# Kernel tuning notes

Hardware: AMD Instinct MI355X
Metric: run time of the kernel (lower is better)

The kernel has to match this reference:

```python
import jax, jax.numpy as jnp
import numpy as np

DEPTH = 3
MAX_NB = 10
HIDDEN = 128


def setup_inputs() -> dict:
    key = jax.random.key(0)
    k = jax.random.split(key, 14)
    B, A, E, H, NB = 64, 1024, 2048, HIDDEN, MAX_NB
    s = 0.05
    return {
        "input_atom": jax.random.normal(k[0], (B, A, 82), jnp.float32),
        "input_bond": jax.random.normal(k[1], (B, E, 6), jnp.float32),
        "atom_graph": jax.random.randint(k[2], (B, A, NB), 0, A),
        "bond_graph": jax.random.randint(k[3], (B, A, NB), 0, E),
        "num_nbs": jax.random.randint(k[4], (B, A), 0, NB + 1),
        "node_mask": jnp.ones((B, A), jnp.float32),
        "W_atom": jax.random.normal(k[5], (82, H), jnp.float32) * s,
        "W_nei_atom": jax.random.normal(k[6], (H, H), jnp.float32) * s,
        "W_nei_bond": jax.random.normal(k[7], (6, H), jnp.float32) * s,
        "W_self": jax.random.normal(k[8], (H, H), jnp.float32) * s,
        "W_U2": jax.random.normal(k[9], (H + 6, H), jnp.float32) * s,
        "b_U2": jax.random.normal(k[10], (H,), jnp.float32) * s,
        "W_U1": jax.random.normal(k[11], (2 * H, H), jnp.float32) * s,
        "b_U1": jax.random.normal(k[12], (H,), jnp.float32) * s,
    }


def reference(input_atom, input_bond, atom_graph, bond_graph, num_nbs, node_mask,
              W_atom, W_nei_atom, W_nei_bond, W_self, W_U2, b_U2, W_U1, b_U1):
    B, A, NB = atom_graph.shape
    H = W_atom.shape[1]
    atom_features = input_atom @ W_atom                       # [B, A, H]
    # neighbor validity mask: [B, A, NB, 1]
    mask_nei = (jnp.arange(NB)[None, None, :] < num_nbs[:, :, None]).astype(jnp.float32)[..., None]
    idx_a = atom_graph.reshape(B, A * NB, 1)
    idx_b = bond_graph.reshape(B, A * NB, 1)
    # bond neighbor features are loop-invariant: gather once
    fbond_nei = jnp.take_along_axis(input_bond, idx_b, axis=1).reshape(B, A, NB, 6)
    h_nei_bond = fbond_nei @ W_nei_bond                       # [B, A, NB, H]
    node_m = node_mask[..., None]                             # [B, A, 1]
    kernel = None
    for _ in range(DEPTH):
        fatom_nei = jnp.take_along_axis(atom_features, idx_a, axis=1).reshape(B, A, NB, H)
        h_nei = (fatom_nei @ W_nei_atom) * h_nei_bond         # [B, A, NB, H]
        f_nei = jnp.sum(h_nei * mask_nei, axis=2)             # [B, A, H]
        f_self = atom_features @ W_self                        # [B, A, H]
        kernel = f_nei * f_self * node_m
        l_nei = jnp.concatenate([fatom_nei, fbond_nei], axis=3)  # [B, A, NB, H+6]
        pre_label = l_nei @ W_U2 + b_U2
        nei_label = jnp.sum(pre_label * mask_nei, axis=2)      # [B, A, H]
        new_label = jnp.concatenate([atom_features, nei_label], axis=2)
        atom_features = new_label @ W_U1 + b_U1
    return kernel, atom_features
```

## Files before the change

### kernel.cpp

```cpp
#include <hip/hip_runtime.h>

constexpr int NB = 10, H = 128;
constexpr int M = 64 * 1024;
constexpr long SL = (long)M * H;

typedef __attribute__((ext_vector_type(8))) short s16x8;
typedef __attribute__((ext_vector_type(4))) float f32x4;

__device__ __forceinline__ ushort f2b(float f) {
    union { float f; uint u; } v; v.f = f;
    uint u = v.u;
    uint r = u + 0x7fffu + ((u >> 16) & 1u);
    return (ushort)(r >> 16);
}
__device__ __forceinline__ float b2f(ushort u) {
    union { uint u; float f; } v; v.u = ((uint)u) << 16; return v.f;
}

__device__ __forceinline__ int swz(int bid, int cpx) {
    return (bid & 7) * cpx + (bid >> 3);
}

template<int NC, int FLAGS>
__global__ __launch_bounds__(256, 4) void gemm_af(
    const ushort* __restrict__ Abf, const ushort* __restrict__ WT,
    const ushort* __restrict__ FNb, const float* __restrict__ nmask,
    float* __restrict__ Cf, ushort* __restrict__ Cb)
{
    constexpr bool KOUT = FLAGS & 8, OF32 = FLAGS & 16;
    constexpr int K = NC * 32;
    const int lane = threadIdx.x & 63, wid = threadIdx.x >> 6;
    const int l15 = lane & 15, g = lane >> 4;
    const int t0 = swz(blockIdx.x, 128) * 4;

    s16x8 w[2][NC];
    #pragma unroll
    for (int ct = 0; ct < 2; ++ct)
        #pragma unroll
        for (int kc = 0; kc < NC; ++kc)
            w[ct][kc] = *(const s16x8*)(WT + (size_t)((2 * wid + ct) * 16 + l15) * K + kc * 32 + g * 8);

    s16x8 ac[NC], an[NC];
    #pragma unroll
    for (int kc = 0; kc < NC; ++kc)
        ac[kc] = *(const s16x8*)(Abf + (size_t)(t0 * 16 + l15) * K + kc * 32 + g * 8);

    #pragma unroll
    for (int i = 0; i < 4; ++i) {
        const int m0 = (t0 + i) * 16;
        if (i < 3) {
            #pragma unroll
            for (int kc = 0; kc < NC; ++kc)
                an[kc] = *(const s16x8*)(Abf + (size_t)(m0 + 16 + l15) * K + kc * 32 + g * 8);
        }
        f32x4 acc[2];
        #pragma unroll
        for (int ct = 0; ct < 2; ++ct) acc[ct] = (f32x4){0.f, 0.f, 0.f, 0.f};
        #pragma unroll
        for (int kc = 0; kc < NC; ++kc)
            #pragma unroll
            for (int ct = 0; ct < 2; ++ct)
                acc[ct] = __builtin_amdgcn_mfma_f32_16x16x32_bf16(ac[kc], w[ct][kc], acc[ct], 0, 0, 0);

        #pragma unroll
        for (int ct = 0; ct < 2; ++ct) {
            const int col = (2 * wid + ct) * 16 + l15;
            #pragma unroll
            for (int r = 0; r < 4; ++r) {
                const int m = m0 + 4 * g + r;
                const size_t o = (size_t)m * H + col;
                float v = acc[ct][r];
                if constexpr (KOUT) v = v * b2f(FNb[o]) * nmask[m];
                if constexpr (OF32) Cf[o] = v; else Cb[o] = f2b(v);
            }
        }
        #pragma unroll
        for (int kc = 0; kc < NC; ++kc) ac[kc] = an[kc];
    }
}

template<bool OF32>
__global__ __launch_bounds__(256, 2) void u1f(
    const ushort* __restrict__ AF, const ushort* __restrict__ SATOM,
    const ushort* __restrict__ FBSb, const ushort* __restrict__ WT,
    float* __restrict__ Cf, ushort* __restrict__ Cb)
{
    const int lane = threadIdx.x & 63, wid = threadIdx.x >> 6;
    const int l15 = lane & 15, g = lane >> 4;
    const int t0 = swz(blockIdx.x, 128) * 4;

    s16x8 w[2][9];
    #pragma unroll
    for (int ct = 0; ct < 2; ++ct)
        #pragma unroll
        for (int kc = 0; kc < 9; ++kc)
            w[ct][kc] = *(const s16x8*)(WT + (size_t)((2 * wid + ct) * 16 + l15) * 288 + kc * 32 + g * 8);

    s16x8 ac[9], an[9];
    {
        const size_t rb = (size_t)(t0 * 16 + l15) * H + g * 8;
        #pragma unroll
        for (int kc = 0; kc < 4; ++kc) {
            ac[kc]     = *(const s16x8*)(AF    + rb + kc * 32);
            ac[kc + 4] = *(const s16x8*)(SATOM + rb + kc * 32);
        }
        ac[8] = (s16x8){0,0,0,0,0,0,0,0};
        if (g == 0) ac[8] = *(const s16x8*)(FBSb + (size_t)(t0 * 16 + l15) * 8);
    }

    #pragma unroll
    for (int i = 0; i < 4; ++i) {
        const int m0 = (t0 + i) * 16;
        if (i < 3) {
            const size_t rb = (size_t)(m0 + 16 + l15) * H + g * 8;
            #pragma unroll
            for (int kc = 0; kc < 4; ++kc) {
                an[kc]     = *(const s16x8*)(AF    + rb + kc * 32);
                an[kc + 4] = *(const s16x8*)(SATOM + rb + kc * 32);
            }
            an[8] = (s16x8){0,0,0,0,0,0,0,0};
            if (g == 0) an[8] = *(const s16x8*)(FBSb + (size_t)(m0 + 16 + l15) * 8);
        }
        f32x4 acc[2];
        #pragma unroll
        for (int ct = 0; ct < 2; ++ct) acc[ct] = (f32x4){0.f, 0.f, 0.f, 0.f};
        #pragma unroll
        for (int kc = 0; kc < 9; ++kc)
            #pragma unroll
            for (int ct = 0; ct < 2; ++ct)
                acc[ct] = __builtin_amdgcn_mfma_f32_16x16x32_bf16(ac[kc], w[ct][kc], acc[ct], 0, 0, 0);

        #pragma unroll
        for (int ct = 0; ct < 2; ++ct) {
            const int col = (2 * wid + ct) * 16 + l15;
            #pragma unroll
            for (int r = 0; r < 4; ++r) {
                const size_t o = (size_t)(m0 + 4 * g + r) * H + col;
                if constexpr (OF32) Cf[o] = acc[ct][r]; else Cb[o] = f2b(acc[ct][r]);
            }
        }
        #pragma unroll
        for (int kc = 0; kc < 9; ++kc) ac[kc] = an[kc];
    }
}

__global__ __launch_bounds__(256, 6) void gather_satom(
    const ushort* __restrict__ AF, const int* __restrict__ ag,
    const int* __restrict__ nn, ushort* __restrict__ SATOM)
{
    const int bid = swz(blockIdx.x, 512);
    const int m  = bid * 16 + (threadIdx.x >> 4);
    const int c8 = (threadIdx.x & 15) * 8;
    const int b  = m >> 10;
    const int nnb = nn[m];
    const ushort* AFb = AF + ((size_t)b << 10) * H + c8;
    const int* agm = ag + (size_t)m * NB;

    int2 iv0 = *(const int2*)(agm + 0);
    int2 iv1 = *(const int2*)(agm + 2);
    int2 iv2 = *(const int2*)(agm + 4);
    int2 iv3 = *(const int2*)(agm + 6);
    int2 iv4 = *(const int2*)(agm + 8);

    float sacc[8];
    #pragma unroll
    for (int i = 0; i < 8; ++i) sacc[i] = 0.f;

    #define GS_STEP(nb, ia)                                              \
    {                                                                    \
        const float w = ((nb) < nnb) ? 1.f : 0.f;                        \
        s16x8 av = *(const s16x8*)(AFb + (size_t)(ia) * H);              \
        _Pragma("unroll")                                                \
        for (int i = 0; i < 8; ++i) sacc[i] += w * b2f((ushort)av[i]);   \
    }
    GS_STEP(0, iv0.x) GS_STEP(1, iv0.y)
    GS_STEP(2, iv1.x) GS_STEP(3, iv1.y)
    GS_STEP(4, iv2.x) GS_STEP(5, iv2.y)
    GS_STEP(6, iv3.x) GS_STEP(7, iv3.y)
    GS_STEP(8, iv4.x) GS_STEP(9, iv4.y)
    #undef GS_STEP

    s16x8 so;
    #pragma unroll
    for (int i = 0; i < 8; ++i) so[i] = (short)f2b(sacc[i]);
    *(s16x8*)(SATOM + (size_t)m * H + c8) = so;
}

__global__ __launch_bounds__(256, 4) void gather_last(
    const ushort* __restrict__ AF, const ushort* __restrict__ ATW,
    const ushort* __restrict__ HB, const int* __restrict__ ag,
    const int* __restrict__ bg, const int* __restrict__ nn,
    ushort* __restrict__ SATOM, ushort* __restrict__ FNEIb)
{
    const int bid = swz(blockIdx.x, 512);
    const int m  = bid * 16 + (threadIdx.x >> 4);
    const int c8 = (threadIdx.x & 15) * 8;
    const int b  = m >> 10;
    const int nnb = nn[m];
    const ushort* AFb  = AF  + ((size_t)b << 10) * H + c8;
    const ushort* ATWb = ATW + ((size_t)b << 10) * H + c8;
    const ushort* HBb  = HB  + ((size_t)b << 11) * H + c8;
    const int* agm = ag + (size_t)m * NB;
    const int* bgm = bg + (size_t)m * NB;

    int2 ia0 = *(const int2*)(agm + 0), ib0 = *(const int2*)(bgm + 0);
    int2 ia1 = *(const int2*)(agm + 2), ib1 = *(const int2*)(bgm + 2);
    int2 ia2 = *(const int2*)(agm + 4), ib2 = *(const int2*)(bgm + 4);
    int2 ia3 = *(const int2*)(agm + 6), ib3 = *(const int2*)(bgm + 6);
    int2 ia4 = *(const int2*)(agm + 8), ib4 = *(const int2*)(bgm + 8);

    float sacc[8], facc[8];
    #pragma unroll
    for (int i = 0; i < 8; ++i) { sacc[i] = 0.f; facc[i] = 0.f; }

    #define GL_STEP(nb, ia, ib)                                          \
    {                                                                    \
        const float w = ((nb) < nnb) ? 1.f : 0.f;                        \
        s16x8 av = *(const s16x8*)(AFb  + (size_t)(ia) * H);             \
        s16x8 tv = *(const s16x8*)(ATWb + (size_t)(ia) * H);             \
        s16x8 hv = *(const s16x8*)(HBb  + (size_t)(ib) * H);             \
        _Pragma("unroll")                                                \
        for (int i = 0; i < 8; ++i) {                                    \
            sacc[i] += w * b2f((ushort)av[i]);                           \
            facc[i] += (w * b2f((ushort)tv[i])) * b2f((ushort)hv[i]);    \
        }                                                                \
    }
    GL_STEP(0, ia0.x, ib0.x) GL_STEP(1, ia0.y, ib0.y)
    GL_STEP(2, ia1.x, ib1.x) GL_STEP(3, ia1.y, ib1.y)
    GL_STEP(4, ia2.x, ib2.x) GL_STEP(5, ia2.y, ib2.y)
    GL_STEP(6, ia3.x, ib3.x) GL_STEP(7, ia3.y, ib3.y)
    GL_STEP(8, ia4.x, ib4.x) GL_STEP(9, ia4.y, ib4.y)
    #undef GL_STEP

    s16x8 so, fo;
    #pragma unroll
    for (int i = 0; i < 8; ++i) { so[i] = (short)f2b(sacc[i]); fo[i] = (short)f2b(facc[i]); }
    *(s16x8*)(SATOM + (size_t)m * H + c8) = so;
    *(s16x8*)(FNEIb + (size_t)m * H + c8) = fo;
}

__global__ __launch_bounds__(256) void prep_hb(
    const float* __restrict__ bond, const float* __restrict__ Wnb,
    ushort* __restrict__ HB)
{
    const int t = blockIdx.x * 256 + threadIdx.x;
    const int r = t >> 4, c8 = (t & 15) * 8;
    const float* fb = bond + (size_t)r * 6;
    const float2 f01 = *(const float2*)fb;
    const float2 f23 = *(const float2*)(fb + 2);
    const float2 f45 = *(const float2*)(fb + 4);
    s16x8 o;
    #pragma unroll
    for (int i = 0; i < 8; ++i) {
        const int c = c8 + i;
        const float v = f01.x * Wnb[0 * H + c] + f01.y * Wnb[1 * H + c]
                      + f23.x * Wnb[2 * H + c] + f23.y * Wnb[3 * H + c]
                      + f45.x * Wnb[4 * H + c] + f45.y * Wnb[5 * H + c];
        o[i] = (short)f2b(v);
    }
    *(s16x8*)(HB + (size_t)r * H + c8) = o;
}

__global__ __launch_bounds__(256) void prep_fbs(
    const float* __restrict__ bond, const int* __restrict__ bg,
    const int* __restrict__ nn, ushort* __restrict__ FBSb)
{
    const int m = blockIdx.x * 256 + threadIdx.x;
    const int b = m >> 10;
    const int nnb = nn[m];
    float s[6] = {0,0,0,0,0,0};
    for (int nb = 0; nb < nnb; ++nb) {
        const int ib = bg[m * NB + nb];
        const float* fb = bond + ((size_t)(b << 11) + (size_t)ib) * 6;
        #pragma unroll
        for (int j = 0; j < 6; ++j) s[j] += fb[j];
    }
    s16x8 o;
    #pragma unroll
    for (int j = 0; j < 6; ++j) o[j] = (short)f2b(s[j]);
    o[6] = (short)f2b((float)nnb);
    o[7] = (short)f2b(1.0f);
    *(s16x8*)(FBSb + (size_t)m * 8) = o;
}

__global__ __launch_bounds__(256) void cvt_atom(
    const float* __restrict__ ia, ushort* __restrict__ out)
{
    const int tid = blockIdx.x * 256 + threadIdx.x;
    const int m = tid / 12, c = (tid % 12) * 8;
    s16x8 v;
    #pragma unroll
    for (int i = 0; i < 8; ++i) {
        const int k = c + i;
        v[i] = (short)(k < 82 ? f2b(ia[(size_t)m * 82 + k]) : 0);
    }
    *(s16x8*)(out + (size_t)m * 96 + c) = v;
}

__global__ __launch_bounds__(256) void prep_w(
    const float* __restrict__ Wa, const float* __restrict__ Wna,
    const float* __restrict__ Ws, const float* __restrict__ Wu2,
    const float* __restrict__ bu2, const float* __restrict__ Wu1,
    const float* __restrict__ bu1, ushort* __restrict__ out)
{
    int t = blockIdx.x * 256 + threadIdx.x;
    const int tid = t;
    if (t < 128 * 96) { int n = t / 96, k = t % 96;
        out[tid] = (k < 82) ? f2b(Wa[k * H + n]) : 0; return; }
    t -= 128 * 96;
    if (t < 128 * 128) { int n = t / 128, k = t % 128;
        out[tid] = f2b(Wna[k * H + n]); return; }
    t -= 128 * 128;
    if (t < 128 * 128) { int n = t / 128, k = t % 128;
        out[tid] = f2b(Ws[k * H + n]); return; }
    t -= 128 * 128;
    if (t < 128 * 288) {
        const int n = t / 288, k = t % 288;
        float v = 0.f;
        if (k < 128) {
            v = Wu1[k * H + n];
        } else if (k < 256) {
            const int kk = k - 128;
            float s = 0.f;
            for (int j = 0; j < 128; ++j) s += Wu2[kk * H + j] * Wu1[(128 + j) * H + n];
            v = s;
        } else {
            const int j = k - 256;
            if (j < 6) {
                float s = 0.f;
                for (int q = 0; q < 128; ++q) s += Wu2[(128 + j) * H + q] * Wu1[(128 + q) * H + n];
                v = s;
            } else if (j == 6) {
                float s = 0.f;
                for (int q = 0; q < 128; ++q) s += bu2[q] * Wu1[(128 + q) * H + n];
                v = s;
            } else if (j == 7) {
                v = bu1[n];
            }
        }
        out[tid] = f2b(v);
        return;
    }
}

extern "C" void kernel_launch(void* const* d_in, const int* in_sizes, int n_in,
                              void* d_out, int out_size, void* d_ws, size_t ws_size,
                              hipStream_t stream)
{
    (void)in_sizes; (void)n_in; (void)out_size; (void)ws_size;

    const float* input_atom = (const float*)d_in[0];
    const float* input_bond = (const float*)d_in[1];
    const int*   atom_graph = (const int*)d_in[2];
    const int*   bond_graph = (const int*)d_in[3];
    const int*   num_nbs    = (const int*)d_in[4];
    const float* node_mask  = (const float*)d_in[5];
    const float* W_atom     = (const float*)d_in[6];
    const float* W_nei_atom = (const float*)d_in[7];
    const float* W_nei_bond = (const float*)d_in[8];
    const float* W_self     = (const float*)d_in[9];
    const float* W_U2       = (const float*)d_in[10];
    const float* b_U2       = (const float*)d_in[11];
    const float* W_U1       = (const float*)d_in[12];
    const float* b_U1       = (const float*)d_in[13];

    char* ws = (char*)d_ws;
    ushort* AF0   = (ushort*)(ws);
    ushort* AF1   = (ushort*)(ws + SL * 2);
    ushort* SATw  = (ushort*)(ws + SL * 4);
    ushort* ATW   = SATw;
    ushort* HB    = (ushort*)(ws + SL * 6);
    ushort* AFin  = (ushort*)(ws + SL * 6);
    ushort* FBSb  = (ushort*)(ws + SL * 10);
    ushort* WTs_  = (ushort*)(ws + SL * 10 + (size_t)M * 8 * 2);

    ushort* WTa   = WTs_;
    ushort* WTna  = WTa   + 128 * 96;
    ushort* WTslf = WTna  + 128 * 128;
    ushort* WTu1f = WTslf + 128 * 128;

    float*  out0  = (float*)d_out;
    float*  out1  = out0 + SL;
    ushort* SATl  = (ushort*)out0;
    ushort* FNEIb = AF1;

    prep_w<<<320, 256, 0, stream>>>(W_atom, W_nei_atom, W_self, W_U2, b_U2,
                                    W_U1, b_U1, WTs_);
    cvt_atom<<<3072, 256, 0, stream>>>(input_atom, AFin);
    prep_fbs<<<256, 256, 0, stream>>>(input_bond, bond_graph, num_nbs, FBSb);

    gemm_af<3, 0><<<1024, 256, 0, stream>>>(AFin, WTa, nullptr, nullptr,
                                            nullptr, AF0);

    gather_satom<<<4096, 256, 0, stream>>>(AF0, atom_graph, num_nbs, SATw);
    u1f<false><<<1024, 256, 0, stream>>>(AF0, SATw, FBSb, WTu1f, nullptr, AF1);
    gather_satom<<<4096, 256, 0, stream>>>(AF1, atom_graph, num_nbs, SATw);
    u1f<false><<<1024, 256, 0, stream>>>(AF1, SATw, FBSb, WTu1f, nullptr, AF0);

    gemm_af<4, 0><<<1024, 256, 0, stream>>>(AF0, WTna, nullptr, nullptr,
                                            nullptr, ATW);
    prep_hb<<<8192, 256, 0, stream>>>(input_bond, W_nei_bond, HB);
    gather_last<<<4096, 256, 0, stream>>>(AF0, ATW, HB, atom_graph, bond_graph,
                                          num_nbs, SATl, FNEIb);
    u1f<true><<<1024, 256, 0, stream>>>(AF0, SATl, FBSb, WTu1f, out1, nullptr);
    gemm_af<4, 8 | 16><<<1024, 256, 0, stream>>>(AF0, WTslf, FNEIb, node_mask,
                                                 out0, nullptr);
}
```

Measured before the change: 216.9 us.

## Merge prep kernels and final GEMMs, branch-skip masked neighbors, drop A prefetch

Folds the four prep kernels (weights, bond sums, atom conversion, bond projection) into one launch. Merges the final U1 GEMM and the self-kernel GEMM into one grid split by block index, which needs SATl moved out of out0 into its own workspace buffer. Gathers now skip the loads for masked neighbors with a branch instead of multiplying them by zero. GEMM bodies drop the double-buffered A prefetch and raise occupancy hints to cut register pressure and launch overhead, at the risk of less latency hiding.

```diff
diff --git a/kernel.cpp b/kernel.cpp
--- a/kernel.cpp
+++ b/kernel.cpp
@@ -22,8 +22,8 @@
 }
 
 template<int NC, int FLAGS>
-__global__ __launch_bounds__(256, 4) void gemm_af(
-    const ushort* __restrict__ Abf, const ushort* __restrict__ WT,
+__device__ __forceinline__ void gemm_body(
+    int tg, const ushort* __restrict__ Abf, const ushort* __restrict__ WT,
     const ushort* __restrict__ FNb, const float* __restrict__ nmask,
     float* __restrict__ Cf, ushort* __restrict__ Cb)
 {
@@ -31,7 +31,6 @@
     constexpr int K = NC * 32;
     const int lane = threadIdx.x & 63, wid = threadIdx.x >> 6;
     const int l15 = lane & 15, g = lane >> 4;
-    const int t0 = swz(blockIdx.x, 128) * 4;
 
     s16x8 w[2][NC];
     #pragma unroll
@@ -40,19 +39,14 @@
         for (int kc = 0; kc < NC; ++kc)
             w[ct][kc] = *(const s16x8*)(WT + (size_t)((2 * wid + ct) * 16 + l15) * K + kc * 32 + g * 8);
 
-    s16x8 ac[NC], an[NC];
-    #pragma unroll
-    for (int kc = 0; kc < NC; ++kc)
-        ac[kc] = *(const s16x8*)(Abf + (size_t)(t0 * 16 + l15) * K + kc * 32 + g * 8);
-
     #pragma unroll
     for (int i = 0; i < 4; ++i) {
-        const int m0 = (t0 + i) * 16;
-        if (i < 3) {
-            #pragma unroll
-            for (int kc = 0; kc < NC; ++kc)
-                an[kc] = *(const s16x8*)(Abf + (size_t)(m0 + 16 + l15) * K + kc * 32 + g * 8);
-        }
+        const int m0 = (tg * 4 + i) * 16;
+        s16x8 ac[NC];
+        #pragma unroll
+        for (int kc = 0; kc < NC; ++kc)
+            ac[kc] = *(const s16x8*)(Abf + (size_t)(m0 + l15) * K + kc * 32 + g * 8);
+
         f32x4 acc[2];
         #pragma unroll
         for (int ct = 0; ct < 2; ++ct) acc[ct] = (f32x4){0.f, 0.f, 0.f, 0.f};
@@ -74,20 +68,17 @@
                 if constexpr (OF32) Cf[o] = v; else Cb[o] = f2b(v);
             }
         }
-        #pragma unroll
-        for (int kc = 0; kc < NC; ++kc) ac[kc] = an[kc];
     }
 }
 
 template<bool OF32>
-__global__ __launch_bounds__(256, 2) void u1f(
-    const ushort* __restrict__ AF, const ushort* __restrict__ SATOM,
+__device__ __forceinline__ void u1f_body(
+    int tg, const ushort* __restrict__ AF, const ushort* __restrict__ SATOM,
     const ushort* __restrict__ FBSb, const ushort* __restrict__ WT,
     float* __restrict__ Cf, ushort* __restrict__ Cb)
 {
     const int lane = threadIdx.x & 63, wid = threadIdx.x >> 6;
     const int l15 = lane & 15, g = lane >> 4;
-    const int t0 = swz(blockIdx.x, 128) * 4;
 
     s16x8 w[2][9];
     #pragma unroll
@@ -96,31 +87,19 @@
         for (int kc = 0; kc < 9; ++kc)
             w[ct][kc] = *(const s16x8*)(WT + (size_t)((2 * wid + ct) * 16 + l15) * 288 + kc * 32 + g * 8);
 
-    s16x8 ac[9], an[9];
-    {
-        const size_t rb = (size_t)(t0 * 16 + l15) * H + g * 8;
+    #pragma unroll
+    for (int i = 0; i < 4; ++i) {
+        const int m0 = (tg * 4 + i) * 16;
+        const size_t rb = (size_t)(m0 + l15) * H + g * 8;
+        s16x8 ac[9];
         #pragma unroll
         for (int kc = 0; kc < 4; ++kc) {
             ac[kc]     = *(const s16x8*)(AF    + rb + kc * 32);
             ac[kc + 4] = *(const s16x8*)(SATOM + rb + kc * 32);
         }
         ac[8] = (s16x8){0,0,0,0,0,0,0,0};
-        if (g == 0) ac[8] = *(const s16x8*)(FBSb + (size_t)(t0 * 16 + l15) * 8);
-    }
-
-    #pragma unroll
-    for (int i = 0; i < 4; ++i) {
-        const int m0 = (t0 + i) * 16;
-        if (i < 3) {
-            const size_t rb = (size_t)(m0 + 16 + l15) * H + g * 8;
-            #pragma unroll
-            for (int kc = 0; kc < 4; ++kc) {
-                an[kc]     = *(const s16x8*)(AF    + rb + kc * 32);
-                an[kc + 4] = *(const s16x8*)(SATOM + rb + kc * 32);
-            }
-            an[8] = (s16x8){0,0,0,0,0,0,0,0};
-            if (g == 0) an[8] = *(const s16x8*)(FBSb + (size_t)(m0 + 16 + l15) * 8);
-        }
+        if (g == 0) ac[8] = *(const s16x8*)(FBSb + (size_t)(m0 + l15) * 8);
+
         f32x4 acc[2];
         #pragma unroll
         for (int ct = 0; ct < 2; ++ct) acc[ct] = (f32x4){0.f, 0.f, 0.f, 0.f};
@@ -139,12 +118,42 @@
                 if constexpr (OF32) Cf[o] = acc[ct][r]; else Cb[o] = f2b(acc[ct][r]);
             }
         }
-        #pragma unroll
-        for (int kc = 0; kc < 9; ++kc) ac[kc] = an[kc];
     }
 }
 
-__global__ __launch_bounds__(256, 6) void gather_satom(
+template<int NC, int FLAGS>
+__global__ __launch_bounds__(256, 4) void gemm_af(
+    const ushort* __restrict__ Abf, const ushort* __restrict__ WT,
+    const ushort* __restrict__ FNb, const float* __restrict__ nmask,
+    float* __restrict__ Cf, ushort* __restrict__ Cb)
+{
+    gemm_body<NC, FLAGS>(swz(blockIdx.x, 128), Abf, WT, FNb, nmask, Cf, Cb);
+}
+
+template<bool OF32>
+__global__ __launch_bounds__(256, 4) void u1f(
+    const ushort* __restrict__ AF, const ushort* __restrict__ SATOM,
+    const ushort* __restrict__ FBSb, const ushort* __restrict__ WT,
+    float* __restrict__ Cf, ushort* __restrict__ Cb)
+{
+    u1f_body<OF32>(swz(blockIdx.x, 128), AF, SATOM, FBSb, WT, Cf, Cb);
+}
+
+__global__ __launch_bounds__(256, 4) void final2(
+    const ushort* __restrict__ AF, const ushort* __restrict__ SATl,
+    const ushort* __restrict__ FBSb, const ushort* __restrict__ WTu1f,
+    const ushort* __restrict__ WTslf, const ushort* __restrict__ FNEIb,
+    const float* __restrict__ nmask, float* __restrict__ out1,
+    float* __restrict__ out0)
+{
+    if (blockIdx.x < 1024)
+        u1f_body<true>(swz(blockIdx.x, 128), AF, SATl, FBSb, WTu1f, out1, nullptr);
+    else
+        gemm_body<4, 8 | 16>(swz(blockIdx.x - 1024, 128), AF, WTslf, FNEIb,
+                             nmask, out0, nullptr);
+}
+
+__global__ __launch_bounds__(256, 8) void gather_satom(
     const ushort* __restrict__ AF, const int* __restrict__ ag,
     const int* __restrict__ nn, ushort* __restrict__ SATOM)
 {
@@ -167,11 +176,10 @@
     for (int i = 0; i < 8; ++i) sacc[i] = 0.f;
 
     #define GS_STEP(nb, ia)                                              \
-    {                                                                    \
-        const float w = ((nb) < nnb) ? 1.f : 0.f;                        \
+    if ((nb) < nnb) {                                                    \
         s16x8 av = *(const s16x8*)(AFb + (size_t)(ia) * H);              \
         _Pragma("unroll")                                                \
-        for (int i = 0; i < 8; ++i) sacc[i] += w * b2f((ushort)av[i]);   \
+        for (int i = 0; i < 8; ++i) sacc[i] += b2f((ushort)av[i]);       \
     }
     GS_STEP(0, iv0.x) GS_STEP(1, iv0.y)
     GS_STEP(2, iv1.x) GS_STEP(3, iv1.y)
@@ -214,15 +222,14 @@
     for (int i = 0; i < 8; ++i) { sacc[i] = 0.f; facc[i] = 0.f; }
 
     #define GL_STEP(nb, ia, ib)                                          \
-    {                                                                    \
-        const float w = ((nb) < nnb) ? 1.f : 0.f;                        \
+    if ((nb) < nnb) {                                                    \
         s16x8 av = *(const s16x8*)(AFb  + (size_t)(ia) * H);             \
         s16x8 tv = *(const s16x8*)(ATWb + (size_t)(ia) * H);             \
         s16x8 hv = *(const s16x8*)(HBb  + (size_t)(ib) * H);             \
         _Pragma("unroll")                                                \
         for (int i = 0; i < 8; ++i) {                                    \
-            sacc[i] += w * b2f((ushort)av[i]);                           \
-            facc[i] += (w * b2f((ushort)tv[i])) * b2f((ushort)hv[i]);    \
+            sacc[i] += b2f((ushort)av[i]);                               \
+            facc[i] += b2f((ushort)tv[i]) * b2f((ushort)hv[i]);          \
         }                                                                \
     }
     GL_STEP(0, ia0.x, ib0.x) GL_STEP(1, ia0.y, ib0.y)
@@ -239,107 +246,100 @@
     *(s16x8*)(FNEIb + (size_t)m * H + c8) = fo;
 }
 
-__global__ __launch_bounds__(256) void prep_hb(
-    const float* __restrict__ bond, const float* __restrict__ Wnb,
-    ushort* __restrict__ HB)
-{
-    const int t = blockIdx.x * 256 + threadIdx.x;
-    const int r = t >> 4, c8 = (t & 15) * 8;
-    const float* fb = bond + (size_t)r * 6;
-    const float2 f01 = *(const float2*)fb;
-    const float2 f23 = *(const float2*)(fb + 2);
-    const float2 f45 = *(const float2*)(fb + 4);
-    s16x8 o;
-    #pragma unroll
-    for (int i = 0; i < 8; ++i) {
-        const int c = c8 + i;
-        const float v = f01.x * Wnb[0 * H + c] + f01.y * Wnb[1 * H + c]
-                      + f23.x * Wnb[2 * H + c] + f23.y * Wnb[3 * H + c]
-                      + f45.x * Wnb[4 * H + c] + f45.y * Wnb[5 * H + c];
-        o[i] = (short)f2b(v);
-    }
-    *(s16x8*)(HB + (size_t)r * H + c8) = o;
-}
-
-__global__ __launch_bounds__(256) void prep_fbs(
-    const float* __restrict__ bond, const int* __restrict__ bg,
-    const int* __restrict__ nn, ushort* __restrict__ FBSb)
-{
-    const int m = blockIdx.x * 256 + threadIdx.x;
-    const int b = m >> 10;
-    const int nnb = nn[m];
-    float s[6] = {0,0,0,0,0,0};
-    for (int nb = 0; nb < nnb; ++nb) {
-        const int ib = bg[m * NB + nb];
-        const float* fb = bond + ((size_t)(b << 11) + (size_t)ib) * 6;
-        #pragma unroll
-        for (int j = 0; j < 6; ++j) s[j] += fb[j];
-    }
-    s16x8 o;
-    #pragma unroll
-    for (int j = 0; j < 6; ++j) o[j] = (short)f2b(s[j]);
-    o[6] = (short)f2b((float)nnb);
-    o[7] = (short)f2b(1.0f);
-    *(s16x8*)(FBSb + (size_t)m * 8) = o;
-}
-
-__global__ __launch_bounds__(256) void cvt_atom(
-    const float* __restrict__ ia, ushort* __restrict__ out)
-{
-    const int tid = blockIdx.x * 256 + threadIdx.x;
-    const int m = tid / 12, c = (tid % 12) * 8;
-    s16x8 v;
-    #pragma unroll
-    for (int i = 0; i < 8; ++i) {
-        const int k = c + i;
-        v[i] = (short)(k < 82 ? f2b(ia[(size_t)m * 82 + k]) : 0);
-    }
-    *(s16x8*)(out + (size_t)m * 96 + c) = v;
-}
-
-__global__ __launch_bounds__(256) void prep_w(
+__global__ __launch_bounds__(256) void prep_all(
     const float* __restrict__ Wa, const float* __restrict__ Wna,
     const float* __restrict__ Ws, const float* __restrict__ Wu2,
     const float* __restrict__ bu2, const float* __restrict__ Wu1,
-    const float* __restrict__ bu1, ushort* __restrict__ out)
-{
-    int t = blockIdx.x * 256 + threadIdx.x;
-    const int tid = t;
-    if (t < 128 * 96) { int n = t / 96, k = t % 96;
-        out[tid] = (k < 82) ? f2b(Wa[k * H + n]) : 0; return; }
-    t -= 128 * 96;
-    if (t < 128 * 128) { int n = t / 128, k = t % 128;
-        out[tid] = f2b(Wna[k * H + n]); return; }
-    t -= 128 * 128;
-    if (t < 128 * 128) { int n = t / 128, k = t % 128;
-        out[tid] = f2b(Ws[k * H + n]); return; }
-    t -= 128 * 128;
-    if (t < 128 * 288) {
-        const int n = t / 288, k = t % 288;
-        float v = 0.f;
-        if (k < 128) {
-            v = Wu1[k * H + n];
-        } else if (k < 256) {
-            const int kk = k - 128;
-            float s = 0.f;
-            for (int j = 0; j < 128; ++j) s += Wu2[kk * H + j] * Wu1[(128 + j) * H + n];
-            v = s;
-        } else {
-            const int j = k - 256;
-            if (j < 6) {
+    const float* __restrict__ bu1, const float* __restrict__ bond,
+    const int* __restrict__ bg, const int* __restrict__ nn,
+    const float* __restrict__ ia, const float* __restrict__ Wnb,
+    ushort* __restrict__ WTs, ushort* __restrict__ FBSb,
+    ushort* __restrict__ AFin, ushort* __restrict__ HB)
+{
+    const int bid = blockIdx.x;
+    if (bid < 320) {
+        int t = bid * 256 + threadIdx.x;
+        const int tid = t;
+        if (t < 128 * 96) { int n = t / 96, k = t % 96;
+            WTs[tid] = (k < 82) ? f2b(Wa[k * H + n]) : 0; return; }
+        t -= 128 * 96;
+        if (t < 128 * 128) { int n = t / 128, k = t % 128;
+            WTs[tid] = f2b(Wna[k * H + n]); return; }
+        t -= 128 * 128;
+        if (t < 128 * 128) { int n = t / 128, k = t % 128;
+            WTs[tid] = f2b(Ws[k * H + n]); return; }
+        t -= 128 * 128;
+        {
+            const int n = t / 288, k = t % 288;
+            float v = 0.f;
+            if (k < 128) {
+                v = Wu1[k * H + n];
+            } else if (k < 256) {
+                const int kk = k - 128;
                 float s = 0.f;
-                for (int q = 0; q < 128; ++q) s += Wu2[(128 + j) * H + q] * Wu1[(128 + q) * H + n];
+                for (int j = 0; j < 128; ++j) s += Wu2[kk * H + j] * Wu1[(128 + j) * H + n];
                 v = s;
-            } else if (j == 6) {
-                float s = 0.f;
-                for (int q = 0; q < 128; ++q) s += bu2[q] * Wu1[(128 + q) * H + n];
-                v = s;
-            } else if (j == 7) {
-                v = bu1[n];
+            } else {
+                const int j = k - 256;
+                if (j < 6) {
+                    float s = 0.f;
+                    for (int q = 0; q < 128; ++q) s += Wu2[(128 + j) * H + q] * Wu1[(128 + q) * H + n];
+                    v = s;
+                } else if (j == 6) {
+                    float s = 0.f;
+                    for (int q = 0; q < 128; ++q) s += bu2[q] * Wu1[(128 + q) * H + n];
+                    v = s;
+                } else if (j == 7) {
+                    v = bu1[n];
+                }
             }
-        }
-        out[tid] = f2b(v);
-        return;
+            WTs[tid] = f2b(v);
+            return;
+        }
+    } else if (bid < 576) {
+        const int m = (bid - 320) * 256 + threadIdx.x;
+        const int b = m >> 10;
+        const int nnb = nn[m];
+        float s[6] = {0,0,0,0,0,0};
+        for (int nb = 0; nb < nnb; ++nb) {
+            const int ib = bg[m * NB + nb];
+            const float* fb = bond + ((size_t)(b << 11) + (size_t)ib) * 6;
+            #pragma unroll
+            for (int j = 0; j < 6; ++j) s[j] += fb[j];
+        }
+        s16x8 o;
+        #pragma unroll
+        for (int j = 0; j < 6; ++j) o[j] = (short)f2b(s[j]);
+        o[6] = (short)f2b((float)nnb);
+        o[7] = (short)f2b(1.0f);
+        *(s16x8*)(FBSb + (size_t)m * 8) = o;
+    } else if (bid < 3648) {
+        const int tid = (bid - 576) * 256 + threadIdx.x;
+        const int m = tid / 12, c = (tid % 12) * 8;
+        s16x8 v;
+        #pragma unroll
+        for (int i = 0; i < 8; ++i) {
+            const int k = c + i;
+            v[i] = (short)(k < 82 ? f2b(ia[(size_t)m * 82 + k]) : 0);
+        }
+        *(s16x8*)(AFin + (size_t)m * 96 + c) = v;
+    } else {
+        const int t = (bid - 3648) * 256 + threadIdx.x;
+        const int r = t >> 4, c8 = (t & 15) * 8;
+        const float* fb = bond + (size_t)r * 6;
+        const float2 f01 = *(const float2*)fb;
+        const float2 f23 = *(const float2*)(fb + 2);
+        const float2 f45 = *(const float2*)(fb + 4);
+        s16x8 o;
+        #pragma unroll
+        for (int i = 0; i < 8; ++i) {
+            const int c = c8 + i;
+            const float v = f01.x * Wnb[0 * H + c] + f01.y * Wnb[1 * H + c]
+                          + f23.x * Wnb[2 * H + c] + f23.y * Wnb[3 * H + c]
+                          + f45.x * Wnb[4 * H + c] + f45.y * Wnb[5 * H + c];
+            o[i] = (short)f2b(v);
+        }
+        *(s16x8*)(HB + (size_t)r * H + c8) = o;
     }
 }
 
@@ -365,14 +365,16 @@
     const float* b_U1       = (const float*)d_in[13];
 
     char* ws = (char*)d_ws;
+    const size_t MB = 1024 * 1024;
     ushort* AF0   = (ushort*)(ws);
-    ushort* AF1   = (ushort*)(ws + SL * 2);
-    ushort* SATw  = (ushort*)(ws + SL * 4);
+    ushort* AF1   = (ushort*)(ws + 16 * MB);
+    ushort* SATw  = (ushort*)(ws + 32 * MB);
     ushort* ATW   = SATw;
-    ushort* HB    = (ushort*)(ws + SL * 6);
-    ushort* AFin  = (ushort*)(ws + SL * 6);
-    ushort* FBSb  = (ushort*)(ws + SL * 10);
-    ushort* WTs_  = (ushort*)(ws + SL * 10 + (size_t)M * 8 * 2);
+    ushort* AFin  = (ushort*)(ws + 48 * MB);
+    ushort* HB    = (ushort*)(ws + 64 * MB);
+    ushort* SATl  = (ushort*)(ws + 96 * MB);
+    ushort* FBSb  = (ushort*)(ws + 112 * MB);
+    ushort* WTs_  = (ushort*)(ws + 113 * MB);
 
     ushort* WTa   = WTs_;
     ushort* WTna  = WTa   + 128 * 96;
@@ -381,13 +383,12 @@
 
     float*  out0  = (float*)d_out;
     float*  out1  = out0 + SL;
-    ushort* SATl  = (ushort*)out0;
     ushort* FNEIb = AF1;
 
-    prep_w<<<320, 256, 0, stream>>>(W_atom, W_nei_atom, W_self, W_U2, b_U2,
-                                    W_U1, b_U1, WTs_);
-    cvt_atom<<<3072, 256, 0, stream>>>(input_atom, AFin);
-    prep_fbs<<<256, 256, 0, stream>>>(input_bond, bond_graph, num_nbs, FBSb);
+    prep_all<<<11840, 256, 0, stream>>>(W_atom, W_nei_atom, W_self, W_U2, b_U2,
+                                        W_U1, b_U1, input_bond, bond_graph,
+                                        num_nbs, input_atom, W_nei_bond,
+                                        WTs_, FBSb, AFin, HB);
 
     gemm_af<3, 0><<<1024, 256, 0, stream>>>(AFin, WTa, nullptr, nullptr,
                                             nullptr, AF0);
@@ -399,10 +400,8 @@
 
     gemm_af<4, 0><<<1024, 256, 0, stream>>>(AF0, WTna, nullptr, nullptr,
                                             nullptr, ATW);
-    prep_hb<<<8192, 256, 0, stream>>>(input_bond, W_nei_bond, HB);
     gather_last<<<4096, 256, 0, stream>>>(AF0, ATW, HB, atom_graph, bond_graph,
                                           num_nbs, SATl, FNEIb);
-    u1f<true><<<1024, 256, 0, stream>>>(AF0, SATl, FBSb, WTu1f, out1, nullptr);
-    gemm_af<4, 8 | 16><<<1024, 256, 0, stream>>>(AF0, WTslf, FNEIb, node_mask,
-                                                 out0, nullptr);
-}
+    final2<<<2048, 256, 0, stream>>>(AF0, SATl, FBSb, WTu1f, WTslf, FNEIb,
+                                     node_mask, out1, out0);
+}
```

Measured after the change: 193.3 us. 1.12x faster.
